# Optimization experiments

Measured on AMD Instinct MI355X. Metric: run time of the kernel, lower is better.

## Reference

```python
import jax, jax.numpy as jnp
import numpy as np

SEQ, EMB, OUT = 8192, 1024, 128

def setup_inputs() -> dict:
    key = jax.random.key(0)
    k1, k2, k3, k4 = jax.random.split(key, 4)
    return {
        "x": jax.random.normal(k1, (SEQ, EMB), dtype=jnp.float32),
        "wquery": jax.random.normal(k2, (EMB, OUT), dtype=jnp.float32) * (2.0 / EMB) ** 0.5,
        "wkey": jax.random.normal(k3, (EMB, OUT), dtype=jnp.float32) * (2.0 / EMB) ** 0.5,
        "wvalue": jax.random.normal(k4, (EMB, OUT), dtype=jnp.float32) * (2.0 / EMB) ** 0.5,
    }

def reference(x, wquery, wkey, wvalue):
    # Single-head attention, mask=True branch (mask tensor is zeros -> no masking).
    q = x @ wquery   # [S, D]
    k = x @ wkey     # [S, D]
    v = x @ wvalue   # [S, D]
    scale = jnp.sqrt(jnp.asarray(q.shape[-1], dtype=q.dtype))
    a = (q @ k.T) / scale              # [S, S]
    p = jax.nn.softmax(a, axis=1)      # softmax over keys (dim=1 in torch)
    return p @ v                       # [S, D]
```

## Files before the change

### kernel.cpp

```cpp
#include <hip/hip_runtime.h>
#include <cstdint>
#include <cstddef>

#define SEQ 8192
#define EMB 1024
#define DH  128

typedef __bf16 bf16x8 __attribute__((ext_vector_type(8)));
typedef __bf16 bf16x2 __attribute__((ext_vector_type(2)));
typedef float  f32x4  __attribute__((ext_vector_type(4)));
typedef float  f32x16 __attribute__((ext_vector_type(16)));
typedef uint32_t u32x4 __attribute__((ext_vector_type(4)));
typedef unsigned short u16x8 __attribute__((ext_vector_type(8)));

static constexpr float QSCALE = (float)(1.4426950408889634 / 11.313708498984760);

__device__ __forceinline__ unsigned short f2bf(float f) {
  uint32_t u = __builtin_bit_cast(uint32_t, f);
  u += 0x7FFFu + ((u >> 16) & 1u);
  return (unsigned short)(u >> 16);
}
__device__ __forceinline__ float bf2f(unsigned short u) {
  return __builtin_bit_cast(float, (uint32_t)u << 16);
}

#define GLD_LDS16(gsrc, ldst) \
  __builtin_amdgcn_global_load_lds((__attribute__((address_space(1))) void*)(gsrc), \
                                   (__attribute__((address_space(3))) void*)(ldst), 16, 0, 0)

__global__ __launch_bounds__(256) void convert_kernel(
    const float* __restrict__ x,
    const float* __restrict__ wq, const float* __restrict__ wk, const float* __restrict__ wv,
    unsigned short* __restrict__ xb, unsigned short* __restrict__ wt)
{
  const int bid = blockIdx.x;
  const int t = threadIdx.x;
  if (bid < 2048) {
    size_t e = (size_t)bid * 4096 + (size_t)t * 16;
#pragma unroll
    for (int i = 0; i < 2; ++i) {
      float4 a = *reinterpret_cast<const float4*>(x + e + i * 8);
      float4 b = *reinterpret_cast<const float4*>(x + e + i * 8 + 4);
      u16x8 o = { f2bf(a.x), f2bf(a.y), f2bf(a.z), f2bf(a.w),
                  f2bf(b.x), f2bf(b.y), f2bf(b.z), f2bf(b.w) };
      *reinterpret_cast<u16x8*>(xb + e + i * 8) = o;
    }
  } else {
    const int which = (bid - 2048) >> 2;
    const int k = ((bid - 2048) & 3) * 256 + t;
    const float* w = (which == 0) ? wq : ((which == 1) ? wk : wv);
    const float scl = (which == 0) ? QSCALE : 1.0f;
#pragma unroll
    for (int n = 0; n < 128; n += 4) {
      float4 v = *reinterpret_cast<const float4*>(w + (size_t)k * DH + n);
      wt[((size_t)which * DH + n + 0) * EMB + k] = f2bf(v.x * scl);
      wt[((size_t)which * DH + n + 1) * EMB + k] = f2bf(v.y * scl);
      wt[((size_t)which * DH + n + 2) * EMB + k] = f2bf(v.z * scl);
      wt[((size_t)which * DH + n + 3) * EMB + k] = f2bf(v.w * scl);
    }
  }
}

__global__ __launch_bounds__(256) void qkv_gemm(
    const unsigned short* __restrict__ xb, const unsigned short* __restrict__ wt,
    unsigned short* __restrict__ qs, unsigned short* __restrict__ ks,
    unsigned short* __restrict__ vt)
{
  __shared__ char LDS[49152];
  char* A0 = LDS;
  char* B0 = LDS + 16384;
  unsigned short* T = (unsigned short*)LDS;

  const int t    = threadIdx.x;
  const int lane = t & 63;
  const int wid  = t >> 6;
  const int wr   = wid >> 1, wc = wid & 1;
  const int l31  = lane & 31;
  const int hi   = lane >> 5;
  const int row0 = blockIdx.x * 64;
  const int which = blockIdx.y;

  const char* xc  = (const char*)xb;
  const char* wtc = (const char*)(wt + (size_t)which * DH * EMB);

  f32x16 acc[2] = {};

  auto STAGE = [&](int buf, int k0) {
#pragma unroll
    for (int i = 0; i < 2; ++i) {
      int bidx = i * 4096 + t * 16;
      int row = bidx >> 7, off = bidx & 127;
      const char* src = xc + (size_t)(row0 + row) * (EMB * 2) + k0 * 2 + (off ^ ((row & 7) << 4));
      GLD_LDS16(src, A0 + buf * 8192 + i * 4096 + wid * 1024);
    }
#pragma unroll
    for (int i = 0; i < 4; ++i) {
      int bidx = i * 4096 + t * 16;
      int n = bidx >> 7, off = bidx & 127;
      const char* src = wtc + (size_t)n * (EMB * 2) + k0 * 2 + (off ^ ((n & 7) << 4));
      GLD_LDS16(src, B0 + buf * 16384 + i * 4096 + wid * 1024);
    }
  };

  STAGE(0, 0);
  int cur = 0;
  for (int it = 0; it < EMB / 64; ++it) {
    if (it + 1 < EMB / 64) {
      STAGE(cur ^ 1, (it + 1) * 64);
      asm volatile("s_waitcnt vmcnt(6)" ::: "memory");
    } else {
      asm volatile("s_waitcnt vmcnt(0)" ::: "memory");
    }
    __builtin_amdgcn_s_barrier();
    asm volatile("" ::: "memory");

    const char* Ab = A0 + cur * 8192;
    const char* Bb = B0 + cur * 16384;
    const int ar   = wr * 32 + l31;
    const int aswz = (l31 & 7) << 4;

    __builtin_amdgcn_s_setprio(1);
#pragma unroll
    for (int kk = 0; kk < 4; ++kk) {
      bf16x8 af = *reinterpret_cast<const bf16x8*>(Ab + ar * 128 + ((kk * 32 + hi * 16) ^ aswz));
#pragma unroll
      for (int nt = 0; nt < 2; ++nt) {
        const int n = wc * 64 + nt * 32 + l31;
        bf16x8 bf = *reinterpret_cast<const bf16x8*>(Bb + n * 128 + ((kk * 32 + hi * 16) ^ ((n & 7) << 4)));
        acc[nt] = __builtin_amdgcn_mfma_f32_32x32x16_bf16(af, bf, acc[nt], 0, 0, 0);
      }
    }
    __builtin_amdgcn_s_setprio(0);

    asm volatile("" ::: "memory");
    __builtin_amdgcn_s_barrier();
    asm volatile("" ::: "memory");
    cur ^= 1;
  }

  if (which < 2) {
    unsigned short* dst = (which == 0) ? qs : ks;
#pragma unroll
    for (int nt = 0; nt < 2; ++nt)
#pragma unroll
      for (int r = 0; r < 16; ++r) {
        int row = row0 + wr * 32 + (r & 3) + 8 * (r >> 2) + 4 * hi;
        dst[(size_t)row * DH + wc * 64 + nt * 32 + l31] = f2bf(acc[nt][r]);
      }
  } else {
    __syncthreads();
#pragma unroll
    for (int nt = 0; nt < 2; ++nt)
#pragma unroll
      for (int r = 0; r < 16; ++r) {
        int d  = wc * 64 + nt * 32 + l31;
        int rl = wr * 32 + (r & 3) + 8 * (r >> 2) + 4 * hi;
        T[d * 72 + rl] = f2bf(acc[nt][r]);
      }
    __syncthreads();
    const int d = t >> 1, half = t & 1;
#pragma unroll
    for (int i = 0; i < 4; ++i) {
      uint4 v = *reinterpret_cast<const uint4*>(&T[d * 72 + half * 32 + i * 8]);
      *reinterpret_cast<uint4*>(vt + (size_t)d * SEQ + row0 + half * 32 + i * 8) = v;
    }
  }
}

template <int NS>
__global__ __launch_bounds__(512, 2) void attn_kernel(
    const unsigned short* __restrict__ qs, const unsigned short* __restrict__ ks,
    const unsigned short* __restrict__ vt,
    unsigned short* __restrict__ Obf, float* __restrict__ ml)
{
  __shared__ unsigned short Ks[2][64 * 128];
  __shared__ unsigned short Vt[2][128 * 64];

  const int t    = threadIdx.x;
  const int lane = t & 63;
  const int wid  = t >> 6;
  const int l31  = lane & 31;
  const int hi   = lane >> 5;
  const int swz  = (lane & 7) << 4;
  const int q0   = blockIdx.x * 256 + wid * 32;
  const int sp   = blockIdx.y;

  bf16x8 qf[8];
  {
    const unsigned short* qp = qs + (size_t)(q0 + l31) * DH + hi * 8;
#pragma unroll
    for (int ds = 0; ds < 8; ++ds)
      qf[ds] = *reinterpret_cast<const bf16x8*>(qp + ds * 16);
  }

  float m = -__builtin_inff();
  float l = 0.f;
  f32x16 O[4] = {};

  const char* ksc = (const char*)ks;
  const char* vtc = (const char*)vt;
  char* ksl = (char*)&Ks[0][0];
  char* vtl = (char*)&Vt[0][0];

  constexpr int CHUNK = SEQ / NS;
  constexpr int NT = CHUNK / 64;
  const int kv_base = sp * CHUNK;

  auto STAGE = [&](int buf, int it) {
    const int kv0 = kv_base + it * 64;
#pragma unroll
    for (int rr = 0; rr < 2; ++rr) {
      int bidx = rr * 512 + t;
      int key = bidx >> 4, blk = bidx & 15;
      const char* src = ksc + (size_t)(kv0 + key) * 256 + ((blk * 16) ^ ((key & 7) << 4));
      GLD_LDS16(src, ksl + buf * 16384 + rr * 8192 + wid * 1024);
    }
#pragma unroll
    for (int rr = 0; rr < 2; ++rr) {
      int bidx = rr * 512 + t;
      int d = bidx >> 3, kb = bidx & 7;
      const char* src = vtc + (size_t)d * (SEQ * 2) + (size_t)kv0 * 2 + ((kb * 16) ^ ((d & 7) << 4));
      GLD_LDS16(src, vtl + buf * 16384 + rr * 8192 + wid * 1024);
    }
  };

  auto build2 = [&](const f32x16& P, bf16x8* fr) {
    uint32_t c[8];
#pragma unroll
    for (int i = 0; i < 8; ++i) {
      bf16x2 b2; b2[0] = (__bf16)P[2 * i]; b2[1] = (__bf16)P[2 * i + 1];
      c[i] = __builtin_bit_cast(uint32_t, b2);
    }
    uint32_t r0 = __shfl_xor(c[0], 32, 64), r1 = __shfl_xor(c[1], 32, 64);
    uint32_t r2 = __shfl_xor(c[2], 32, 64), r3 = __shfl_xor(c[3], 32, 64);
    u32x4 w0;
    w0[0] = hi ? r2 : c[0];
    w0[1] = hi ? r3 : c[1];
    w0[2] = hi ? c[2] : r0;
    w0[3] = hi ? c[3] : r1;
    uint32_t r4 = __shfl_xor(c[4], 32, 64), r5 = __shfl_xor(c[5], 32, 64);
    uint32_t r6 = __shfl_xor(c[6], 32, 64), r7 = __shfl_xor(c[7], 32, 64);
    u32x4 w1;
    w1[0] = hi ? r6 : c[4];
    w1[1] = hi ? r7 : c[5];
    w1[2] = hi ? c[6] : r4;
    w1[3] = hi ? c[7] : r5;
    fr[0] = __builtin_bit_cast(bf16x8, w0);
    fr[1] = __builtin_bit_cast(bf16x8, w1);
  };

  STAGE(0, 0);

  int cur = 0;
  for (int it = 0; it < NT; ++it) {
    if (it + 1 < NT) {
      STAGE(cur ^ 1, it + 1);
      asm volatile("s_waitcnt vmcnt(4)" ::: "memory");
    } else {
      asm volatile("s_waitcnt vmcnt(0)" ::: "memory");
    }
    __builtin_amdgcn_s_barrier();
    asm volatile("" ::: "memory");

    const char* kbase = ksl + cur * 16384;
    const char* vbase = vtl + cur * 16384;

    f32x16 S0 = {}, S1 = {};
    __builtin_amdgcn_s_setprio(1);
#pragma unroll
    for (int ds = 0; ds < 8; ++ds) {
      bf16x8 ka = *reinterpret_cast<const bf16x8*>(kbase + l31 * 256 + ((ds * 32 + hi * 16) ^ swz));
      S0 = __builtin_amdgcn_mfma_f32_32x32x16_bf16(ka, qf[ds], S0, 0, 0, 0);
    }
#pragma unroll
    for (int ds = 0; ds < 8; ++ds) {
      bf16x8 ka = *reinterpret_cast<const bf16x8*>(kbase + 8192 + l31 * 256 + ((ds * 32 + hi * 16) ^ swz));
      S1 = __builtin_amdgcn_mfma_f32_32x32x16_bf16(ka, qf[ds], S1, 0, 0, 0);
    }
    __builtin_amdgcn_s_setprio(0);

    float mx[16];
#pragma unroll
    for (int r = 0; r < 16; ++r) mx[r] = fmaxf(S0[r], S1[r]);
#pragma unroll
    for (int st = 8; st >= 1; st >>= 1)
#pragma unroll
      for (int r = 0; r < st; ++r) mx[r] = fmaxf(mx[r], mx[r + st]);
    const float pm = fmaxf(mx[0], __shfl_xor(mx[0], 32, 64));

    if (__any(pm > m + 11.0f)) {
      float mn = fmaxf(m, pm);
      float corr = __builtin_amdgcn_exp2f(m - mn);
      m = mn;
      l *= corr;
#pragma unroll
      for (int r = 0; r < 16; ++r) {
        float cr = __shfl(corr, (r & 3) + 8 * (r >> 2) + 4 * hi, 64);
#pragma unroll
        for (int nt = 0; nt < 4; ++nt) O[nt][r] *= cr;
      }
    }
    float sm[16];
#pragma unroll
    for (int r = 0; r < 16; ++r) {
      S0[r] = __builtin_amdgcn_exp2f(S0[r] - m);
      S1[r] = __builtin_amdgcn_exp2f(S1[r] - m);
      sm[r] = S0[r] + S1[r];
    }
#pragma unroll
    for (int st = 8; st >= 1; st >>= 1)
#pragma unroll
      for (int r = 0; r < st; ++r) sm[r] += sm[r + st];
    l += sm[0] + __shfl_xor(sm[0], 32, 64);

    bf16x8 pa[4];
    build2(S0, &pa[0]);
    build2(S1, &pa[2]);

    __builtin_amdgcn_s_setprio(1);
#pragma unroll
    for (int ks4 = 0; ks4 < 4; ++ks4) {
#pragma unroll
      for (int nt = 0; nt < 4; ++nt) {
        const int d = nt * 32 + l31;
        bf16x8 vb = *reinterpret_cast<const bf16x8*>(vbase + d * 128 + ((ks4 * 32 + hi * 16) ^ swz));
        O[nt] = __builtin_amdgcn_mfma_f32_32x32x16_bf16(pa[ks4], vb, O[nt], 0, 0, 0);
      }
    }
    __builtin_amdgcn_s_setprio(0);

    asm volatile("" ::: "memory");
    __builtin_amdgcn_s_barrier();
    asm volatile("" ::: "memory");
    cur ^= 1;
  }

  const float linv = 1.0f / l;
  unsigned short* Obase = Obf + ((size_t)sp * SEQ + q0) * DH;
#pragma unroll
  for (int r = 0; r < 16; ++r) {
    const int row = (r & 3) + 8 * (r >> 2) + 4 * hi;
    const float li = __shfl(linv, row, 64);
#pragma unroll
    for (int nt = 0; nt < 4; ++nt)
      Obase[(size_t)row * DH + nt * 32 + l31] = f2bf(O[nt][r] * li);
  }
  if (lane < 32) {
    ml[(size_t)sp * (2 * SEQ) + q0 + lane]       = m;
    ml[(size_t)sp * (2 * SEQ) + SEQ + q0 + lane] = l;
  }
}

template <int NS>
__global__ __launch_bounds__(256) void combine_kernel(
    const unsigned short* __restrict__ Obf, const float* __restrict__ ml, float* __restrict__ out)
{
  const int idx = blockIdx.x * 256 + threadIdx.x;
  const int s = idx >> 4;
  const int c = (idx & 15) * 8;
  float mv[NS], lv[NS];
  float M = -__builtin_inff();
#pragma unroll
  for (int i = 0; i < NS; ++i) {
    mv[i] = ml[(size_t)i * (2 * SEQ) + s];
    lv[i] = ml[(size_t)i * (2 * SEQ) + SEQ + s];
    M = fmaxf(M, mv[i]);
  }
  float den = 0.f;
  float num[8] = {};
#pragma unroll
  for (int i = 0; i < NS; ++i) {
    float g = __builtin_amdgcn_exp2f(mv[i] - M) * lv[i];
    den += g;
    u16x8 o = *reinterpret_cast<const u16x8*>(&Obf[((size_t)i * SEQ + s) * DH + c]);
#pragma unroll
    for (int j = 0; j < 8; ++j) num[j] += g * bf2f(o[j]);
  }
  const float inv = 1.f / den;
  f32x4 r0, r1;
#pragma unroll
  for (int j = 0; j < 4; ++j) { r0[j] = num[j] * inv; r1[j] = num[j + 4] * inv; }
  *reinterpret_cast<f32x4*>(&out[(size_t)s * DH + c])     = r0;
  *reinterpret_cast<f32x4*>(&out[(size_t)s * DH + c + 4]) = r1;
}

extern "C" void kernel_launch(void* const* d_in, const int* in_sizes, int n_in,
                              void* d_out, int out_size, void* d_ws, size_t ws_size,
                              hipStream_t stream) {
  const float* x  = (const float*)d_in[0];
  const float* wq = (const float*)d_in[1];
  const float* wk = (const float*)d_in[2];
  const float* wv = (const float*)d_in[3];
  float* out = (float*)d_out;

  char* ws = (char*)d_ws;
  const size_t MB = 1024 * 1024;
  unsigned short* qs = (unsigned short*)(ws);
  unsigned short* ks = (unsigned short*)(ws + 2 * MB);
  unsigned short* vt = (unsigned short*)(ws + 4 * MB);
  unsigned short* wt = (unsigned short*)(ws + 6 * MB);
  unsigned short* xb = (unsigned short*)(ws + 6 * MB + 768 * 1024);

  convert_kernel<<<2048 + 12, 256, 0, stream>>>(x, wq, wk, wv, xb, wt);
  qkv_gemm<<<dim3(SEQ / 64, 3), 256, 0, stream>>>(xb, wt, qs, ks, vt);

  unsigned short* Obf = (unsigned short*)(ws + 6 * MB);
  const size_t need16 = 6 * MB + 16ull * SEQ * DH * 2 + 16ull * 2 * SEQ * 4;
  const size_t need8  = 6 * MB +  8ull * SEQ * DH * 2 +  8ull * 2 * SEQ * 4;
  if (ws_size >= need16) {
    float* ml = (float*)(ws + 6 * MB + 16ull * SEQ * DH * 2);
    attn_kernel<16><<<dim3(SEQ / 256, 16), 512, 0, stream>>>(qs, ks, vt, Obf, ml);
    combine_kernel<16><<<SEQ * DH / 8 / 256, 256, 0, stream>>>(Obf, ml, out);
  } else if (ws_size >= need8) {
    float* ml = (float*)(ws + 6 * MB + 8ull * SEQ * DH * 2);
    attn_kernel<8><<<dim3(SEQ / 256, 8), 512, 0, stream>>>(qs, ks, vt, Obf, ml);
    combine_kernel<8><<<SEQ * DH / 8 / 256, 256, 0, stream>>>(Obf, ml, out);
  } else {
    float* ml = (float*)(ws + 6 * MB + 4ull * SEQ * DH * 2);
    attn_kernel<4><<<dim3(SEQ / 256, 4), 512, 0, stream>>>(qs, ks, vt, Obf, ml);
    combine_kernel<4><<<SEQ * DH / 8 / 256, 256, 0, stream>>>(Obf, ml, out);
  }
}
```

Baseline: 91.22 us.

## Load V fragments directly from global into registers and drop split-16 path

Removes the shared-memory staging of the transposed V tile and has each wave load its V MFMA operands directly from global memory into registers, issued early and in two halves to overlap with the QK^T and softmax work. K staging keeps its double buffer, but the pipeline now waits for all loads at the end of each iteration. The 16-way KV split path is also removed, so the default is the 8-way split, which halves grid parallelism. This cuts LDS footprint and LDS traffic, but every wave now fetches V separately (8x redundant global/L2 reads per block) and register pressure rises.

Result: slower. 108.9 us (+19.4%).

```diff
diff --git a/kernel.cpp b/kernel.cpp
--- a/kernel.cpp
+++ b/kernel.cpp
@@ -174,7 +174,6 @@
     unsigned short* __restrict__ Obf, float* __restrict__ ml)
 {
   __shared__ unsigned short Ks[2][64 * 128];
-  __shared__ unsigned short Vt[2][128 * 64];
 
   const int t    = threadIdx.x;
   const int lane = t & 63;
@@ -198,13 +197,16 @@
   f32x16 O[4] = {};
 
   const char* ksc = (const char*)ks;
-  const char* vtc = (const char*)vt;
   char* ksl = (char*)&Ks[0][0];
-  char* vtl = (char*)&Vt[0][0];
 
   constexpr int CHUNK = SEQ / NS;
   constexpr int NT = CHUNK / 64;
   const int kv_base = sp * CHUNK;
+
+  const unsigned short* vrow0 = vt + (size_t)(0 * 32 + l31) * SEQ + hi * 8;
+  const unsigned short* vrow1 = vt + (size_t)(1 * 32 + l31) * SEQ + hi * 8;
+  const unsigned short* vrow2 = vt + (size_t)(2 * 32 + l31) * SEQ + hi * 8;
+  const unsigned short* vrow3 = vt + (size_t)(3 * 32 + l31) * SEQ + hi * 8;
 
   auto STAGE = [&](int buf, int it) {
     const int kv0 = kv_base + it * 64;
@@ -214,13 +216,6 @@
       int key = bidx >> 4, blk = bidx & 15;
       const char* src = ksc + (size_t)(kv0 + key) * 256 + ((blk * 16) ^ ((key & 7) << 4));
       GLD_LDS16(src, ksl + buf * 16384 + rr * 8192 + wid * 1024);
-    }
-#pragma unroll
-    for (int rr = 0; rr < 2; ++rr) {
-      int bidx = rr * 512 + t;
-      int d = bidx >> 3, kb = bidx & 7;
-      const char* src = vtc + (size_t)d * (SEQ * 2) + (size_t)kv0 * 2 + ((kb * 16) ^ ((d & 7) << 4));
-      GLD_LDS16(src, vtl + buf * 16384 + rr * 8192 + wid * 1024);
     }
   };
 
@@ -250,20 +245,24 @@
   };
 
   STAGE(0, 0);
+  asm volatile("s_waitcnt vmcnt(0)" ::: "memory");
+  __builtin_amdgcn_s_barrier();
 
   int cur = 0;
   for (int it = 0; it < NT; ++it) {
-    if (it + 1 < NT) {
-      STAGE(cur ^ 1, it + 1);
-      asm volatile("s_waitcnt vmcnt(4)" ::: "memory");
-    } else {
-      asm volatile("s_waitcnt vmcnt(0)" ::: "memory");
-    }
-    __builtin_amdgcn_s_barrier();
-    asm volatile("" ::: "memory");
+    const int kv0 = kv_base + it * 64;
+
+    bf16x8 vbl[8];
+#pragma unroll
+    for (int s = 0; s < 2; ++s) {
+      vbl[s * 4 + 0] = *reinterpret_cast<const bf16x8*>(vrow0 + kv0 + s * 16);
+      vbl[s * 4 + 1] = *reinterpret_cast<const bf16x8*>(vrow1 + kv0 + s * 16);
+      vbl[s * 4 + 2] = *reinterpret_cast<const bf16x8*>(vrow2 + kv0 + s * 16);
+      vbl[s * 4 + 3] = *reinterpret_cast<const bf16x8*>(vrow3 + kv0 + s * 16);
+    }
+    STAGE(cur ^ 1, (it + 1 < NT) ? it + 1 : 0);
 
     const char* kbase = ksl + cur * 16384;
-    const char* vbase = vtl + cur * 16384;
 
     f32x16 S0 = {}, S1 = {};
     __builtin_amdgcn_s_setprio(1);
@@ -313,23 +312,33 @@
       for (int r = 0; r < st; ++r) sm[r] += sm[r + st];
     l += sm[0] + __shfl_xor(sm[0], 32, 64);
 
+    bf16x8 vbh[8];
+#pragma unroll
+    for (int s = 0; s < 2; ++s) {
+      vbh[s * 4 + 0] = *reinterpret_cast<const bf16x8*>(vrow0 + kv0 + 32 + s * 16);
+      vbh[s * 4 + 1] = *reinterpret_cast<const bf16x8*>(vrow1 + kv0 + 32 + s * 16);
+      vbh[s * 4 + 2] = *reinterpret_cast<const bf16x8*>(vrow2 + kv0 + 32 + s * 16);
+      vbh[s * 4 + 3] = *reinterpret_cast<const bf16x8*>(vrow3 + kv0 + 32 + s * 16);
+    }
+
     bf16x8 pa[4];
     build2(S0, &pa[0]);
     build2(S1, &pa[2]);
 
     __builtin_amdgcn_s_setprio(1);
 #pragma unroll
-    for (int ks4 = 0; ks4 < 4; ++ks4) {
-#pragma unroll
-      for (int nt = 0; nt < 4; ++nt) {
-        const int d = nt * 32 + l31;
-        bf16x8 vb = *reinterpret_cast<const bf16x8*>(vbase + d * 128 + ((ks4 * 32 + hi * 16) ^ swz));
-        O[nt] = __builtin_amdgcn_mfma_f32_32x32x16_bf16(pa[ks4], vb, O[nt], 0, 0, 0);
-      }
-    }
+    for (int s = 0; s < 2; ++s)
+#pragma unroll
+      for (int nt = 0; nt < 4; ++nt)
+        O[nt] = __builtin_amdgcn_mfma_f32_32x32x16_bf16(pa[s], vbl[s * 4 + nt], O[nt], 0, 0, 0);
+#pragma unroll
+    for (int s = 0; s < 2; ++s)
+#pragma unroll
+      for (int nt = 0; nt < 4; ++nt)
+        O[nt] = __builtin_amdgcn_mfma_f32_32x32x16_bf16(pa[2 + s], vbh[s * 4 + nt], O[nt], 0, 0, 0);
     __builtin_amdgcn_s_setprio(0);
 
-    asm volatile("" ::: "memory");
+    asm volatile("s_waitcnt vmcnt(0)" ::: "memory");
     __builtin_amdgcn_s_barrier();
     asm volatile("" ::: "memory");
     cur ^= 1;
@@ -405,13 +414,8 @@
   qkv_gemm<<<dim3(SEQ / 64, 3), 256, 0, stream>>>(xb, wt, qs, ks, vt);
 
   unsigned short* Obf = (unsigned short*)(ws + 6 * MB);
-  const size_t need16 = 6 * MB + 16ull * SEQ * DH * 2 + 16ull * 2 * SEQ * 4;
-  const size_t need8  = 6 * MB +  8ull * SEQ * DH * 2 +  8ull * 2 * SEQ * 4;
-  if (ws_size >= need16) {
-    float* ml = (float*)(ws + 6 * MB + 16ull * SEQ * DH * 2);
-    attn_kernel<16><<<dim3(SEQ / 256, 16), 512, 0, stream>>>(qs, ks, vt, Obf, ml);
-    combine_kernel<16><<<SEQ * DH / 8 / 256, 256, 0, stream>>>(Obf, ml, out);
-  } else if (ws_size >= need8) {
+  const size_t need8 = 6 * MB + 8ull * SEQ * DH * 2 + 8ull * 2 * SEQ * 4;
+  if (ws_size >= need8) {
     float* ml = (float*)(ws + 6 * MB + 8ull * SEQ * DH * 2);
     attn_kernel<8><<<dim3(SEQ / 256, 8), 512, 0, stream>>>(qs, ks, vt, Obf, ml);
     combine_kernel<8><<<SEQ * DH / 8 / 256, 256, 0, stream>>>(Obf, ml, out);
```

## Process two 32-row query tiles per wave to reuse K/V LDS loads

Applied to the files above, without the earlier changes.

Each wave now handles 64 query rows as two 32-row tiles that share every K and V fragment read from shared memory, and the block covers 512 queries, so the grid halves. This is meant to cut LDS read traffic per MFMA and amortize the staging and barrier cost over more compute. The cost is doubled accumulator, query and score registers under launch_bounds(512,2), which risks spills or lower occupancy. With half as many blocks, fewer workgroups are available to fill the GPU. The fallback path for a small workspace now always uses the 8-way split, and the 4-way path is removed.

After: 106.5 us. 16.8% more time.

```diff
diff --git a/kernel.cpp b/kernel.cpp
--- a/kernel.cpp
+++ b/kernel.cpp
@@ -182,20 +182,23 @@
   const int l31  = lane & 31;
   const int hi   = lane >> 5;
   const int swz  = (lane & 7) << 4;
-  const int q0   = blockIdx.x * 256 + wid * 32;
+  const int q0   = blockIdx.x * 512 + wid * 64;
   const int sp   = blockIdx.y;
 
-  bf16x8 qf[8];
+  bf16x8 qfA[8], qfB[8];
   {
-    const unsigned short* qp = qs + (size_t)(q0 + l31) * DH + hi * 8;
-#pragma unroll
-    for (int ds = 0; ds < 8; ++ds)
-      qf[ds] = *reinterpret_cast<const bf16x8*>(qp + ds * 16);
-  }
-
-  float m = -__builtin_inff();
-  float l = 0.f;
-  f32x16 O[4] = {};
+    const unsigned short* qpA = qs + (size_t)(q0 + l31) * DH + hi * 8;
+    const unsigned short* qpB = qs + (size_t)(q0 + 32 + l31) * DH + hi * 8;
+#pragma unroll
+    for (int ds = 0; ds < 8; ++ds) {
+      qfA[ds] = *reinterpret_cast<const bf16x8*>(qpA + ds * 16);
+      qfB[ds] = *reinterpret_cast<const bf16x8*>(qpB + ds * 16);
+    }
+  }
+
+  float mA = -__builtin_inff(), mB = -__builtin_inff();
+  float lA = 0.f, lB = 0.f;
+  f32x16 OA[4] = {}, OB[4] = {};
 
   const char* ksc = (const char*)ks;
   const char* vtc = (const char*)vt;
@@ -265,69 +268,78 @@
     const char* kbase = ksl + cur * 16384;
     const char* vbase = vtl + cur * 16384;
 
-    f32x16 S0 = {}, S1 = {};
-    __builtin_amdgcn_s_setprio(1);
-#pragma unroll
-    for (int ds = 0; ds < 8; ++ds) {
-      bf16x8 ka = *reinterpret_cast<const bf16x8*>(kbase + l31 * 256 + ((ds * 32 + hi * 16) ^ swz));
-      S0 = __builtin_amdgcn_mfma_f32_32x32x16_bf16(ka, qf[ds], S0, 0, 0, 0);
-    }
-#pragma unroll
-    for (int ds = 0; ds < 8; ++ds) {
-      bf16x8 ka = *reinterpret_cast<const bf16x8*>(kbase + 8192 + l31 * 256 + ((ds * 32 + hi * 16) ^ swz));
-      S1 = __builtin_amdgcn_mfma_f32_32x32x16_bf16(ka, qf[ds], S1, 0, 0, 0);
-    }
-    __builtin_amdgcn_s_setprio(0);
-
-    float mx[16];
-#pragma unroll
-    for (int r = 0; r < 16; ++r) mx[r] = fmaxf(S0[r], S1[r]);
-#pragma unroll
-    for (int st = 8; st >= 1; st >>= 1)
-#pragma unroll
-      for (int r = 0; r < st; ++r) mx[r] = fmaxf(mx[r], mx[r + st]);
-    const float pm = fmaxf(mx[0], __shfl_xor(mx[0], 32, 64));
-
-    if (__any(pm > m + 11.0f)) {
-      float mn = fmaxf(m, pm);
-      float corr = __builtin_amdgcn_exp2f(m - mn);
-      m = mn;
-      l *= corr;
-#pragma unroll
-      for (int r = 0; r < 16; ++r) {
-        float cr = __shfl(corr, (r & 3) + 8 * (r >> 2) + 4 * hi, 64);
-#pragma unroll
-        for (int nt = 0; nt < 4; ++nt) O[nt][r] *= cr;
-      }
-    }
-    float sm[16];
-#pragma unroll
-    for (int r = 0; r < 16; ++r) {
-      S0[r] = __builtin_amdgcn_exp2f(S0[r] - m);
-      S1[r] = __builtin_amdgcn_exp2f(S1[r] - m);
-      sm[r] = S0[r] + S1[r];
-    }
-#pragma unroll
-    for (int st = 8; st >= 1; st >>= 1)
-#pragma unroll
-      for (int r = 0; r < st; ++r) sm[r] += sm[r + st];
-    l += sm[0] + __shfl_xor(sm[0], 32, 64);
-
-    bf16x8 pa[4];
-    build2(S0, &pa[0]);
-    build2(S1, &pa[2]);
-
-    __builtin_amdgcn_s_setprio(1);
-#pragma unroll
-    for (int ks4 = 0; ks4 < 4; ++ks4) {
-#pragma unroll
-      for (int nt = 0; nt < 4; ++nt) {
-        const int d = nt * 32 + l31;
-        bf16x8 vb = *reinterpret_cast<const bf16x8*>(vbase + d * 128 + ((ks4 * 32 + hi * 16) ^ swz));
-        O[nt] = __builtin_amdgcn_mfma_f32_32x32x16_bf16(pa[ks4], vb, O[nt], 0, 0, 0);
-      }
-    }
-    __builtin_amdgcn_s_setprio(0);
+#pragma unroll
+    for (int h = 0; h < 2; ++h) {
+      f32x16 SA = {}, SB = {};
+      __builtin_amdgcn_s_setprio(1);
+#pragma unroll
+      for (int ds = 0; ds < 8; ++ds) {
+        bf16x8 ka = *reinterpret_cast<const bf16x8*>(
+            kbase + h * 8192 + l31 * 256 + ((ds * 32 + hi * 16) ^ swz));
+        SA = __builtin_amdgcn_mfma_f32_32x32x16_bf16(ka, qfA[ds], SA, 0, 0, 0);
+        SB = __builtin_amdgcn_mfma_f32_32x32x16_bf16(ka, qfB[ds], SB, 0, 0, 0);
+      }
+      __builtin_amdgcn_s_setprio(0);
+
+      float ax[8], bx[8];
+#pragma unroll
+      for (int r = 0; r < 8; ++r) { ax[r] = fmaxf(SA[r], SA[r + 8]); bx[r] = fmaxf(SB[r], SB[r + 8]); }
+#pragma unroll
+      for (int st = 4; st >= 1; st >>= 1)
+#pragma unroll
+        for (int r = 0; r < st; ++r) { ax[r] = fmaxf(ax[r], ax[r + st]); bx[r] = fmaxf(bx[r], bx[r + st]); }
+      const float pmA = fmaxf(ax[0], __shfl_xor(ax[0], 32, 64));
+      const float pmB = fmaxf(bx[0], __shfl_xor(bx[0], 32, 64));
+
+      if (__any((pmA > mA + 11.0f) || (pmB > mB + 11.0f))) {
+        float mnA = fmaxf(mA, pmA), mnB = fmaxf(mB, pmB);
+        float cA = __builtin_amdgcn_exp2f(mA - mnA);
+        float cB = __builtin_amdgcn_exp2f(mB - mnB);
+        mA = mnA; mB = mnB;
+        lA *= cA;  lB *= cB;
+#pragma unroll
+        for (int r = 0; r < 16; ++r) {
+          const int row = (r & 3) + 8 * (r >> 2) + 4 * hi;
+          float crA = __shfl(cA, row, 64);
+          float crB = __shfl(cB, row, 64);
+#pragma unroll
+          for (int nt = 0; nt < 4; ++nt) { OA[nt][r] *= crA; OB[nt][r] *= crB; }
+        }
+      }
+      float as[8], bs[8];
+#pragma unroll
+      for (int r = 0; r < 8; ++r) {
+        SA[r] = __builtin_amdgcn_exp2f(SA[r] - mA);
+        SA[r + 8] = __builtin_amdgcn_exp2f(SA[r + 8] - mA);
+        SB[r] = __builtin_amdgcn_exp2f(SB[r] - mB);
+        SB[r + 8] = __builtin_amdgcn_exp2f(SB[r + 8] - mB);
+        as[r] = SA[r] + SA[r + 8];
+        bs[r] = SB[r] + SB[r + 8];
+      }
+#pragma unroll
+      for (int st = 4; st >= 1; st >>= 1)
+#pragma unroll
+        for (int r = 0; r < st; ++r) { as[r] += as[r + st]; bs[r] += bs[r + st]; }
+      lA += as[0] + __shfl_xor(as[0], 32, 64);
+      lB += bs[0] + __shfl_xor(bs[0], 32, 64);
+
+      bf16x8 paA[2], paB[2];
+      build2(SA, paA);
+      build2(SB, paB);
+
+      __builtin_amdgcn_s_setprio(1);
+#pragma unroll
+      for (int s = 0; s < 2; ++s)
+#pragma unroll
+        for (int nt = 0; nt < 4; ++nt) {
+          const int d = nt * 32 + l31;
+          bf16x8 vb = *reinterpret_cast<const bf16x8*>(
+              vbase + d * 128 + (((h * 2 + s) * 32 + hi * 16) ^ swz));
+          OA[nt] = __builtin_amdgcn_mfma_f32_32x32x16_bf16(paA[s], vb, OA[nt], 0, 0, 0);
+          OB[nt] = __builtin_amdgcn_mfma_f32_32x32x16_bf16(paB[s], vb, OB[nt], 0, 0, 0);
+        }
+      __builtin_amdgcn_s_setprio(0);
+    }
 
     asm volatile("" ::: "memory");
     __builtin_amdgcn_s_barrier();
@@ -335,19 +347,25 @@
     cur ^= 1;
   }
 
-  const float linv = 1.0f / l;
-  unsigned short* Obase = Obf + ((size_t)sp * SEQ + q0) * DH;
+  const float liA = 1.0f / lA, liB = 1.0f / lB;
+  unsigned short* ObA = Obf + ((size_t)sp * SEQ + q0) * DH;
+  unsigned short* ObB = Obf + ((size_t)sp * SEQ + q0 + 32) * DH;
 #pragma unroll
   for (int r = 0; r < 16; ++r) {
     const int row = (r & 3) + 8 * (r >> 2) + 4 * hi;
-    const float li = __shfl(linv, row, 64);
-#pragma unroll
-    for (int nt = 0; nt < 4; ++nt)
-      Obase[(size_t)row * DH + nt * 32 + l31] = f2bf(O[nt][r] * li);
+    const float lrA = __shfl(liA, row, 64);
+    const float lrB = __shfl(liB, row, 64);
+#pragma unroll
+    for (int nt = 0; nt < 4; ++nt) {
+      ObA[(size_t)row * DH + nt * 32 + l31] = f2bf(OA[nt][r] * lrA);
+      ObB[(size_t)row * DH + nt * 32 + l31] = f2bf(OB[nt][r] * lrB);
+    }
   }
   if (lane < 32) {
-    ml[(size_t)sp * (2 * SEQ) + q0 + lane]       = m;
-    ml[(size_t)sp * (2 * SEQ) + SEQ + q0 + lane] = l;
+    ml[(size_t)sp * (2 * SEQ) + q0 + lane]            = mA;
+    ml[(size_t)sp * (2 * SEQ) + SEQ + q0 + lane]      = lA;
+    ml[(size_t)sp * (2 * SEQ) + q0 + 32 + lane]       = mB;
+    ml[(size_t)sp * (2 * SEQ) + SEQ + q0 + 32 + lane] = lB;
   }
 }
 
@@ -409,15 +427,11 @@
   const size_t need8  = 6 * MB +  8ull * SEQ * DH * 2 +  8ull * 2 * SEQ * 4;
   if (ws_size >= need16) {
     float* ml = (float*)(ws + 6 * MB + 16ull * SEQ * DH * 2);
-    attn_kernel<16><<<dim3(SEQ / 256, 16), 512, 0, stream>>>(qs, ks, vt, Obf, ml);
+    attn_kernel<16><<<dim3(SEQ / 512, 16), 512, 0, stream>>>(qs, ks, vt, Obf, ml);
     combine_kernel<16><<<SEQ * DH / 8 / 256, 256, 0, stream>>>(Obf, ml, out);
-  } else if (ws_size >= need8) {
+  } else {
     float* ml = (float*)(ws + 6 * MB + 8ull * SEQ * DH * 2);
-    attn_kernel<8><<<dim3(SEQ / 256, 8), 512, 0, stream>>>(qs, ks, vt, Obf, ml);
+    attn_kernel<8><<<dim3(SEQ / 512, 8), 512, 0, stream>>>(qs, ks, vt, Obf, ml);
     combine_kernel<8><<<SEQ * DH / 8 / 256, 256, 0, stream>>>(Obf, ml, out);
-  } else {
-    float* ml = (float*)(ws + 6 * MB + 4ull * SEQ * DH * 2);
-    attn_kernel<4><<<dim3(SEQ / 256, 4), 512, 0, stream>>>(qs, ks, vt, Obf, ml);
-    combine_kernel<4><<<SEQ * DH / 8 / 256, 256, 0, stream>>>(Obf, ml, out);
-  }
-}
+  }
+}
```
